# Kernel tuning notes

Measured on AMD Instinct MI355X. Metric: run time of the kernel, lower is better.

Reference implementation:

```python
import jax, jax.numpy as jnp
import numpy as np

B, T = 4096, 256
NX, NU, NY, NB, NA, H = 128, 16, 16, 32, 32, 256


def _lin(key, fan_in, fan_out):
    return jax.random.normal(key, (fan_in, fan_out), jnp.float32) / np.sqrt(fan_in)


def _mlp_res_params(key, din, dout):
    ks = jax.random.split(key, 4)
    return dict(
        rW=_lin(ks[0], din, dout), rb=jnp.zeros((dout,), jnp.float32),
        W1=_lin(ks[1], din, H), b1=jnp.zeros((H,), jnp.float32),
        W2=_lin(ks[2], H, H), b2=jnp.zeros((H,), jnp.float32),
        W3=_lin(ks[3], H, dout), b3=jnp.zeros((dout,), jnp.float32),
    )


def setup_inputs() -> dict:
    key = jax.random.key(0)
    k_up, k_yp, k_uf, k_enc, k_f, k_h = jax.random.split(key, 6)
    inp = {
        'upast': jax.random.normal(k_up, (B, NB, NU), jnp.float32),
        'ypast': jax.random.normal(k_yp, (B, NA, NY), jnp.float32),
        'ufuture': jax.random.normal(k_uf, (B, T, NU), jnp.float32),
    }
    enc = _mlp_res_params(k_enc, NB * NU + NA * NY, NX)
    f = _mlp_res_params(k_f, NX + NU, NX)
    h = _mlp_res_params(k_h, NX, NY)
    for name, p in (('enc', enc), ('f', f), ('h', h)):
        for k, v in p.items():
            inp[f'{name}_{k}'] = v
    return inp


def _mlp_res(x, rW, rb, W1, b1, W2, b2, W3, b3):
    # MLP_res_net: linear skip + 2-hidden-layer tanh MLP
    hid = jnp.tanh(x @ W1 + b1)
    hid = jnp.tanh(hid @ W2 + b2)
    return (x @ rW + rb) + (hid @ W3 + b3)


def reference(upast, ypast, ufuture,
              enc_rW, enc_rb, enc_W1, enc_b1, enc_W2, enc_b2, enc_W3, enc_b3,
              f_rW, f_rb, f_W1, f_b1, f_W2, f_b2, f_W3, f_b3,
              h_rW, h_rb, h_W1, h_b1, h_W2, h_b2, h_W3, h_b3):
    Bq, Tq = ufuture.shape[:2]
    # encoder: flatten+concat past windows -> x0 [B, nx]
    z = jnp.concatenate([upast.reshape(Bq, -1), ypast.reshape(Bq, -1)], axis=-1)
    x0 = _mlp_res(z, enc_rW, enc_rb, enc_W1, enc_b1, enc_W2, enc_b2, enc_W3, enc_b3)

    def step(x, u):
        xu = jnp.concatenate([x, u], axis=-1)
        x_next = _mlp_res(xu, f_rW, f_rb, f_W1, f_b1, f_W2, f_b2, f_W3, f_b3)
        return x_next, x  # store state BEFORE update (matches torch loop)

    _, xf = jax.lax.scan(step, x0, ufuture.swapaxes(0, 1))  # [T, B, nx]
    xf = xf.swapaxes(0, 1).reshape(Bq * Tq, -1)
    y = _mlp_res(xf, h_rW, h_rb, h_W1, h_b1, h_W2, h_b2, h_W3, h_b3)
    return y.reshape(Bq, Tq, -1)
```

## Files before the change

kernel.cpp:

```cpp
#include <hip/hip_runtime.h>
#include <stdint.h>


typedef __attribute__((ext_vector_type(8))) short s8v;
typedef __attribute__((ext_vector_type(8))) _Float16 h8v;
typedef __attribute__((ext_vector_type(4))) float f4v;

__device__ __forceinline__ f4v mfma16(s8v a, s8v b, f4v c) {
  return __builtin_amdgcn_mfma_f32_16x16x32_bf16(a, b, c, 0, 0, 0);
}
__device__ __forceinline__ f4v mfmaH(h8v a, h8v b, f4v c) {
  return __builtin_amdgcn_mfma_f32_16x16x32_f16(a, b, c, 0, 0, 0);
}
__device__ __forceinline__ f4v zero4() { return (f4v){0.f, 0.f, 0.f, 0.f}; }

__device__ __forceinline__ unsigned short f2b(float x) {
  unsigned int u = __builtin_bit_cast(unsigned int, x);
  u += 0x7fffu + ((u >> 16) & 1u);
  return (unsigned short)(u >> 16);
}
__device__ __forceinline__ float b2f(unsigned short h) {
  return __builtin_bit_cast(float, (unsigned int)h << 16);
}
__device__ __forceinline__ unsigned short f2h(float x) {
  return __builtin_bit_cast(unsigned short, (_Float16)x);
}
__device__ __forceinline__ float h2f(unsigned short h) {
  return (float)__builtin_bit_cast(_Float16, h);
}

__device__ __forceinline__ float tanhf_fast(float x) {
  x = fminf(15.f, fmaxf(-15.f, x));
  float e = __expf(2.f * x);
  return (e - 1.f) / (e + 1.f);
}

struct SwzDesc { const float* src; long woff; long dhi; long dlo; int K; int Kp; int N; int mode; };
struct SwzTable { SwzDesc d[12]; long tot_work; };

__global__ void swz_kernel(SwzTable tbl, unsigned short* __restrict__ dst) {
  long gid = (long)blockIdx.x * 256 + threadIdx.x;
  if (gid >= tbl.tot_work) return;
  int i = 11;
  while (i > 0 && gid < tbl.d[i].woff) --i;
  const SwzDesc m = tbl.d[i];
  long local = gid - m.woff;
  int j = (int)(local & 7);
// ... 106 lines not shown
    s8v al = *(const s8v*)(&h2l[c][kk * 32 + g * 8]);
    s8v bh = *(const s8v*)(W3h + (((long)w * 8 + kk) * 64 + l) * 8);
    s8v bl = *(const s8v*)(W3l + (((long)w * 8 + kk) * 64 + l) * 8);
    ac = mfma16(ah, bh, ac);
    ac = mfma16(al, bh, ac);
    ac = mfma16(ah, bl, ac);
  }
  for (int kk = 0; kk < 32; ++kk) {
    const int cb = kk * 32 + g * 8;
    const float* zp = (cb < 512) ? (upast + zrow + cb) : (ypast + zrow + (cb - 512));
    float4 z0 = *(const float4*)zp;
    float4 z1 = *(const float4*)(zp + 4);
    float zz[8] = {z0.x, z0.y, z0.z, z0.w, z1.x, z1.y, z1.z, z1.w};
    s8v ah, al;
#pragma unroll
    for (int q = 0; q < 8; ++q) {
      unsigned short hi = f2b(zz[q]);
      ah[q] = (short)hi; al[q] = (short)f2b(zz[q] - b2f(hi));
    }
    s8v bh = *(const s8v*)(rWh + (((long)w * 32 + kk) * 64 + l) * 8);
    s8v bl = *(const s8v*)(rWl + (((long)w * 32 + kk) * 64 + l) * 8);
    ac = mfma16(ah, bh, ac);
    ac = mfma16(al, bh, ac);
    ac = mfma16(ah, bl, ac);
  }
  {
    const float bias = b3[w * 16 + c] + rb[w * 16 + c];
#pragma unroll
    for (int j = 0; j < 4; ++j)
      xstate[(long)(b0 + g * 4 + j) * 128 + w * 16 + c] = ac[j] + bias;
  }
}

__global__ __launch_bounds__(512, 2)
void recur_kernel(const float* __restrict__ ufut,
                  const unsigned short* __restrict__ W1h, const unsigned short* __restrict__ W1l,
                  const unsigned short* __restrict__ W2h, const unsigned short* __restrict__ W2l,
                  const unsigned short* __restrict__ W3h, const unsigned short* __restrict__ W3l,
                  const unsigned short* __restrict__ rWh, const unsigned short* __restrict__ rWl,
                  const float* __restrict__ b1, const float* __restrict__ b2,
                  const float* __restrict__ b3, const float* __restrict__ rb,
                  float* __restrict__ xstate,
                  unsigned short* __restrict__ xfh, unsigned short* __restrict__ xfl,
                  int t0, int len) {
  __shared__ __align__(16) unsigned short xu_h[16][168], xu_l[16][168];
  __shared__ __align__(16) unsigned short hh[16][264], hl[16][264];
  __shared__ __align__(16) unsigned short w3h_l[32768];
  __shared__ __align__(16) unsigned short w3l_l[32768];
  const int tid = threadIdx.x;
  const int w = tid >> 6, l = tid & 63;
  const int c = l & 15, g = l >> 4;
  const int b0 = blockIdx.x << 4;

  h8v w1h_r[2][5], w1l_r[2][5], w2h_r[2][8], rwh_r[5], rwl_r[5];
#pragma unroll
  for (int ct = 0; ct < 2; ++ct) {
#pragma unroll
    for (int kk = 0; kk < 5; ++kk) {
      w1h_r[ct][kk] = *(const h8v*)(W1h + (((long)(2 * w + ct) * 5 + kk) * 64 + l) * 8);
      w1l_r[ct][kk] = *(const h8v*)(W1l + (((long)(2 * w + ct) * 5 + kk) * 64 + l) * 8);
    }
#pragma unroll
    for (int kk = 0; kk < 8; ++kk)
      w2h_r[ct][kk] = *(const h8v*)(W2h + (((long)(2 * w + ct) * 8 + kk) * 64 + l) * 8);
  }
#pragma unroll
  for (int kk = 0; kk < 5; ++kk) {
    rwh_r[kk] = *(const h8v*)(rWh + (((long)w * 5 + kk) * 64 + l) * 8);
    rwl_r[kk] = *(const h8v*)(rWl + (((long)w * 5 + kk) * 64 + l) * 8);
  }
  for (int i = tid; i < 4096; i += 512) {
    ((h8v*)w3h_l)[i] = ((const h8v*)W3h)[i];
    ((h8v*)w3l_l)[i] = ((const h8v*)W3l)[i];
  }

  const float bbA = b1[(2 * w + 0) * 16 + c], bbB = b1[(2 * w + 1) * 16 + c];
  const float cbA = b2[(2 * w + 0) * 16 + c], cbB = b2[(2 * w + 1) * 16 + c];
  const float dB  = b3[w * 16 + c] + rb[w * 16 + c];

  for (int idx = tid; idx < 2048; idx += 512) {
    int r = idx >> 7, cc = idx & 127;
    float x = xstate[(long)(b0 + r) * 128 + cc];
    _Float16 hi = (_Float16)x;
    xu_h[r][cc] = __builtin_bit_cast(unsigned short, hi);
    xu_l[r][cc] = f2h((x - (float)hi) * 2048.f);
  }
  for (int idx = tid; idx < 16 * 24; idx += 512) {
    int r = idx / 24, cc = 144 + (idx % 24);
    xu_h[r][cc] = 0; xu_l[r][cc] = 0;
  }
  __syncthreads();

  for (int tc = 0; tc < len; ++tc) {
    const int t = t0 + tc;
    h8v w2s[8];
#pragma unroll
    for (int kk = 0; kk < 8; ++kk)
      w2s[kk] = *(const h8v*)(W2l + (((long)(2 * w + 0) * 8 + kk) * 64 + l) * 8);
    if (tid < 256) {
      int r = tid >> 4, cc = tid & 15;
      float uv = ufut[((long)(b0 + r) * 256 + t) * 16 + cc];
      _Float16 hi = (_Float16)uv;
      xu_h[r][128 + cc] = __builtin_bit_cast(unsigned short, hi);
      xu_l[r][128 + cc] = f2h((uv - (float)hi) * 2048.f);
    }
    {
      int r = tid >> 5, cc0 = (tid & 31) * 4;
      long row = ((long)(b0 + r) * len + tc) * 128 + cc0;
      unsigned long long ph =
            (unsigned long long)xu_h[r][cc0 + 0]
          | ((unsigned long long)xu_h[r][cc0 + 1] << 16)
          | ((unsigned long long)xu_h[r][cc0 + 2] << 32)
          | ((unsigned long long)xu_h[r][cc0 + 3] << 48);
      unsigned long long pl =
            (unsigned long long)xu_l[r][cc0 + 0]
          | ((unsigned long long)xu_l[r][cc0 + 1] << 16)
          | ((unsigned long long)xu_l[r][cc0 + 2] << 32)
          | ((unsigned long long)xu_l[r][cc0 + 3] << 48);
      *(unsigned long long*)(xfh + row) = ph;
      *(unsigned long long*)(xfl + row) = pl;
    }
    __syncthreads();
    float v1s[2][4];
#pragma unroll
    for (int ct = 0; ct < 2; ++ct) {
      f4v t1 = zero4(), tl = zero4();
#pragma unroll
      for (int kk = 0; kk < 5; ++kk) {
        h8v ah = *(const h8v*)(&xu_h[c][kk * 32 + g * 8]);
        h8v al = *(const h8v*)(&xu_l[c][kk * 32 + g * 8]);
        t1 = mfmaH(ah, w1h_r[ct][kk], t1);
        tl = mfmaH(al, w1h_r[ct][kk], tl);
        tl = mfmaH(ah, w1l_r[ct][kk], tl);
      }
      const float bb = ct ? bbB : bbA;
#pragma unroll
      for (int j = 0; j < 4; ++j) v1s[ct][j] = t1[j] + tl[j] * 0x1p-11f + bb;
    }
#pragma unroll
    for (int ct = 0; ct < 2; ++ct)
#pragma unroll
      for (int j = 0; j < 4; ++j) {
        float tv = tanhf_fast(v1s[ct][j]);
        _Float16 hi = (_Float16)tv;
        hh[g * 4 + j][(2 * w + ct) * 16 + c] = __builtin_bit_cast(unsigned short, hi);
        hl[g * 4 + j][(2 * w + ct) * 16 + c] = f2h((tv - (float)hi) * 2048.f);
      }
    __syncthreads();
    float v2s[2][4];
#pragma unroll
    for (int ct = 0; ct < 2; ++ct) {
      f4v t1 = zero4(), tl = zero4();
#pragma unroll
      for (int kk = 0; kk < 8; ++kk) {
        h8v ah = *(const h8v*)(&hh[c][kk * 32 + g * 8]);
        h8v al = *(const h8v*)(&hl[c][kk * 32 + g * 8]);
        t1 = mfmaH(ah, w2h_r[ct][kk], t1);
        tl = mfmaH(al, w2h_r[ct][kk], tl);
        tl = mfmaH(ah, w2s[kk], tl);
        if (ct == 0)
          w2s[kk] = *(const h8v*)(W2l + (((long)(2 * w + 1) * 8 + kk) * 64 + l) * 8);
      }
      const float cb = ct ? cbB : cbA;
#pragma unroll
      for (int j = 0; j < 4; ++j) v2s[ct][j] = t1[j] + tl[j] * 0x1p-11f + cb;
    }
    __syncthreads();
#pragma unroll
    for (int ct = 0; ct < 2; ++ct)
#pragma unroll
      for (int j = 0; j < 4; ++j) {
        float tv = tanhf_fast(v2s[ct][j]);
        _Float16 hi = (_Float16)tv;
        hh[g * 4 + j][(2 * w + ct) * 16 + c] = __builtin_bit_cast(unsigned short, hi);
        hl[g * 4 + j][(2 * w + ct) * 16 + c] = f2h((tv - (float)hi) * 2048.f);
      }
    __syncthreads();
    {
      f4v t1 = zero4(), tl = zero4();
#pragma unroll
      for (int kk = 0; kk < 8; ++kk) {
        h8v ah = *(const h8v*)(&hh[c][kk * 32 + g * 8]);
        h8v al = *(const h8v*)(&hl[c][kk * 32 + g * 8]);
        h8v bh = *(const h8v*)(&w3h_l[((w * 8 + kk) * 64 + l) * 8]);
        h8v bl = *(const h8v*)(&w3l_l[((w * 8 + kk) * 64 + l) * 8]);
        t1 = mfmaH(ah, bh, t1);
        tl = mfmaH(al, bh, tl);
        tl = mfmaH(ah, bl, tl);
      }
#pragma unroll
      for (int kk = 0; kk < 5; ++kk) {
        h8v ah = *(const h8v*)(&xu_h[c][kk * 32 + g * 8]);
        h8v al = *(const h8v*)(&xu_l[c][kk * 32 + g * 8]);
        t1 = mfmaH(ah, rwh_r[kk], t1);
        tl = mfmaH(al, rwh_r[kk], tl);
        tl = mfmaH(ah, rwl_r[kk], tl);
      }
      __syncthreads();
#pragma unroll
      for (int j = 0; j < 4; ++j) {
        float xn = t1[j] + tl[j] * 0x1p-11f + dB;
        _Float16 hi = (_Float16)xn;
        xu_h[g * 4 + j][w * 16 + c] = __builtin_bit_cast(unsigned short, hi);
        xu_l[g * 4 + j][w * 16 + c] = f2h((xn - (float)hi) * 2048.f);
      }
    }
    __syncthreads();
  }
  for (int idx = tid; idx < 2048; idx += 512) {
    int r = idx >> 7, cc = idx & 127;
    xstate[(long)(b0 + r) * 128 + cc] = h2f(xu_h[r][cc]) + h2f(xu_l[r][cc]) * 0x1p-11f;
  }
}

__global__ __launch_bounds__(512, 2)
void hnet_kernel(const unsigned short* __restrict__ xfh, const unsigned short* __restrict__ xfl,
                 const unsigned short* __restrict__ W1, const unsigned short* __restrict__ W2,
                 const unsigned short* __restrict__ W3, const unsigned short* __restrict__ rW,
                 const float* __restrict__ b1, const float* __restrict__ b2,
                 const float* __restrict__ b3, const float* __restrict__ rb,
                 float* __restrict__ out, int t0, int len) {
  __shared__ __align__(16) unsigned short h1[64][264];
  __shared__ __align__(16) unsigned short h2[64][264];
  __shared__ float part[4][16][16];
  const int tid = threadIdx.x;
  const int w = tid >> 6, l = tid & 63;
  const int c = l & 15, g = l >> 4;
  const long row0 = (long)blockIdx.x * 64;

  {
    h8v w1f[2][4];
#pragma unroll
    for (int ct = 0; ct < 2; ++ct)
#pragma unroll
      for (int kk = 0; kk < 4; ++kk)
        w1f[ct][kk] = *(const h8v*)(W1 + (((long)(2 * w + ct) * 4 + kk) * 64 + l) * 8);
    const float bbA = b1[(2 * w + 0) * 16 + c], bbB = b1[(2 * w + 1) * 16 + c];
    for (int rt = 0; rt < 4; ++rt) {
      f4v t10 = zero4(), tl0 = zero4(), t11 = zero4(), tl1 = zero4();
#pragma unroll
      for (int kk = 0; kk < 4; ++kk) {
        h8v ah = *(const h8v*)(xfh + (row0 + rt * 16 + c) * 128 + kk * 32 + g * 8);
        h8v al = *(const h8v*)(xfl + (row0 + rt * 16 + c) * 128 + kk * 32 + g * 8);
        t10 = mfmaH(ah, w1f[0][kk], t10);
        tl0 = mfmaH(al, w1f[0][kk], tl0);
        t11 = mfmaH(ah, w1f[1][kk], t11);
        tl1 = mfmaH(al, w1f[1][kk], tl1);
      }
#pragma unroll
      for (int j = 0; j < 4; ++j) {
        h1[rt * 16 + g * 4 + j][(2 * w + 0) * 16 + c] =
            f2h(tanhf_fast(t10[j] + tl0[j] * 0x1p-11f + bbA));
        h1[rt * 16 + g * 4 + j][(2 * w + 1) * 16 + c] =
            f2h(tanhf_fast(t11[j] + tl1[j] * 0x1p-11f + bbB));
      }
    }
  }
  __syncthreads();
  {
    h8v w2f[2][8];
#pragma unroll
    for (int ct = 0; ct < 2; ++ct)
#pragma unroll
      for (int kk = 0; kk < 8; ++kk)
        w2f[ct][kk] = *(const h8v*)(W2 + (((long)(2 * w + ct) * 8 + kk) * 64 + l) * 8);
    const float bbA = b2[(2 * w + 0) * 16 + c], bbB = b2[(2 * w + 1) * 16 + c];
    for (int rt = 0; rt < 4; ++rt) {
      f4v a0 = zero4(), a1 = zero4();
#pragma unroll
      for (int kk = 0; kk < 8; ++kk) {
        h8v a = *(const h8v*)(&h1[rt * 16 + c][kk * 32 + g * 8]);
        a0 = mfmaH(a, w2f[0][kk], a0);
        a1 = mfmaH(a, w2f[1][kk], a1);
      }
#pragma unroll
      for (int j = 0; j < 4; ++j) {
        h2[rt * 16 + g * 4 + j][(2 * w + 0) * 16 + c] = f2h(tanhf_fast(a0[j] + bbA));
        h2[rt * 16 + g * 4 + j][(2 * w + 1) * 16 + c] = f2h(tanhf_fast(a1[j] + bbB));
      }
    }
  }
  __syncthreads();
  {
    const int rt = w & 3, kh = w >> 2;
    f4v t1 = zero4(), tl = zero4();
#pragma unroll
    for (int kk = 0; kk < 4; ++kk) {
      const int kkg = kh * 4 + kk;
      h8v a = *(const h8v*)(&h2[rt * 16 + c][kkg * 32 + g * 8]);
      h8v b = *(const h8v*)(W3 + ((long)(kkg * 64 + l)) * 8);
      t1 = mfmaH(a, b, t1);
    }
#pragma unroll
    for (int kk = 0; kk < 2; ++kk) {
      const int kkg = kh * 2 + kk;
      h8v ah = *(const h8v*)(xfh + (row0 + rt * 16 + c) * 128 + kkg * 32 + g * 8);
      h8v al = *(const h8v*)(xfl + (row0 + rt * 16 + c) * 128 + kkg * 32 + g * 8);
      h8v b = *(const h8v*)(rW + ((long)(kkg * 64 + l)) * 8);
      t1 = mfmaH(ah, b, t1);
      tl = mfmaH(al, b, tl);
    }
    float val[4];
#pragma unroll
    for (int j = 0; j < 4; ++j) val[j] = t1[j] + tl[j] * 0x1p-11f;
    if (w >= 4) {
#pragma unroll
      for (int j = 0; j < 4; ++j) part[rt][g * 4 + j][c] = val[j];
    }
    __syncthreads();
    if (w < 4) {
      const float bias = b3[c] + rb[c];
#pragma unroll
      for (int j = 0; j < 4; ++j) {
        const long grow = row0 + rt * 16 + g * 4 + j;
        const long bq = grow / len;
        const int tq = (int)(grow - bq * len);
        out[(bq * 256 + (t0 + tq)) * 16 + c] = val[j] + part[rt][g * 4 + j][c] + bias;
      }
    }
  }
}

extern "C" void kernel_launch(void* const* d_in, const int* in_sizes, int n_in,
                              void* d_out, int out_size, void* d_ws, size_t ws_size,
                              hipStream_t stream) {
  (void)in_sizes; (void)n_in; (void)out_size;
  const float* upast = (const float*)d_in[0];
  const float* ypast = (const float*)d_in[1];
  const float* ufut  = (const float*)d_in[2];
  const float* e_rW = (const float*)d_in[3];
  const float* e_rb = (const float*)d_in[4];
  const float* e_W1 = (const float*)d_in[5];
  const float* e_b1 = (const float*)d_in[6];
  const float* e_W2 = (const float*)d_in[7];
  const float* e_b2 = (const float*)d_in[8];
  const float* e_W3 = (const float*)d_in[9];
  const float* e_b3 = (const float*)d_in[10];
  const float* f_rW = (const float*)d_in[11];
  const float* f_rb = (const float*)d_in[12];
  const float* f_W1 = (const float*)d_in[13];
  const float* f_b1 = (const float*)d_in[14];
  const float* f_W2 = (const float*)d_in[15];
  const float* f_b2 = (const float*)d_in[16];
  const float* f_W3 = (const float*)d_in[17];
  const float* f_b3 = (const float*)d_in[18];
  const float* h_rW = (const float*)d_in[19];
  const float* h_rb = (const float*)d_in[20];
  const float* h_W1 = (const float*)d_in[21];
  const float* h_b1 = (const float*)d_in[22];
  const float* h_W2 = (const float*)d_in[23];
// ... 30 lines not shown
  unsigned short* wswz = (unsigned short*)d_ws;
  const long WSHORTS = HB + (offs[11] - offs[8]) + (long)Kps[11] * Ns[11];
  const size_t XOFF = ((size_t)WSHORTS * 2 + 4095) & ~(size_t)4095;
  float* xstate = (float*)((char*)d_ws + XOFF);
  const size_t XF0 = XOFF + (2u << 20);
  int c = 64;
  {
    long cmax = ((long)ws_size - (long)XF0) >> 21;
    if (cmax < c) c = (int)cmax;
    if (c < 1) c = 1;
  }
  unsigned short* xfh = (unsigned short*)((char*)d_ws + XF0);
  unsigned short* xfl = (unsigned short*)((char*)d_ws + XF0 + (size_t)c * 1048576);

  const unsigned short* eW1h = wswz + offs[0];          const unsigned short* eW1l = wswz + EA + offs[0];
  const unsigned short* eW2h = wswz + offs[1];          const unsigned short* eW2l = wswz + EA + offs[1];
  const unsigned short* eW3h = wswz + offs[2];          const unsigned short* eW3l = wswz + EA + offs[2];
  const unsigned short* erWh = wswz + offs[3];          const unsigned short* erWl = wswz + EA + offs[3];
  const unsigned short* fW1h = wswz + FB + 0;           const unsigned short* fW1l = wswz + FB + EB + 0;
  const unsigned short* fW2h = wswz + FB + 40960;       const unsigned short* fW2l = wswz + FB + EB + 40960;
  const unsigned short* fW3h = wswz + FB + 106496;      const unsigned short* fW3l = wswz + FB + EB + 106496;
  const unsigned short* frWh = wswz + FB + 139264;      const unsigned short* frWl = wswz + FB + EB + 139264;
  const unsigned short* hW1 = wswz + HB + 0;
  const unsigned short* hW2 = wswz + HB + 32768;
  const unsigned short* hW3 = wswz + HB + 98304;
  const unsigned short* hrW = wswz + HB + 102400;

  swz_kernel<<<(int)((tbl.tot_work + 255) / 256), 256, 0, stream>>>(tbl, wswz);
  enc_kernel<<<256, 512, 0, stream>>>(upast, ypast,
                                      eW1h, eW1l, eW2h, eW2l, eW3h, eW3l, erWh, erWl,
                                      e_b1, e_b2, e_b3, e_rb, xstate);
  for (int t0 = 0; t0 < 256; t0 += c) {
    int len = 256 - t0; if (len > c) len = c;
    recur_kernel<<<256, 512, 0, stream>>>(ufut, fW1h, fW1l, fW2h, fW2l, fW3h, fW3l,
                                          frWh, frWl, f_b1, f_b2, f_b3, f_rb,
                                          xstate, xfh, xfl, t0, len);
    hnet_kernel<<<64 * len, 512, 0, stream>>>(xfh, xfl, hW1, hW2, hW3, hrW,
                                              h_b1, h_b2, h_b3, h_rb, out, t0, len);
  }
}
```

Baseline: 2.920 ms.

## Double-buffer recurrent state and separate hidden buffers to cut barriers per step

The recurrent kernel now double-buffers the state tile and uses separate LDS buffers for the two hidden layers. This removes the intermediate __syncthreads calls, cutting the per-step barriers from five to three. The input u is loaded directly into registers as the last K-chunk instead of going through LDS. Both column tiles' MFMA chains are interleaved, with separate accumulators for independence. W2-low and W3-low are now streamed from global memory each step instead of being kept in registers or LDS, and launch bounds drop to 1 block per SM. Together these trade occupancy and extra global loads for fewer barriers and more instruction-level parallelism on the latency-bound sequential loop.

```diff
diff --git a/kernel.cpp b/kernel.cpp
--- a/kernel.cpp
+++ b/kernel.cpp
@@ -13,6 +13,12 @@
   return __builtin_amdgcn_mfma_f32_16x16x32_f16(a, b, c, 0, 0, 0);
 }
 __device__ __forceinline__ f4v zero4() { return (f4v){0.f, 0.f, 0.f, 0.f}; }
+__device__ __forceinline__ h8v zeroh8() {
+  h8v z;
+#pragma unroll
+  for (int q = 0; q < 8; ++q) z[q] = (_Float16)0.f;
+  return z;
+}
 
 __device__ __forceinline__ unsigned short f2b(float x) {
   unsigned int u = __builtin_bit_cast(unsigned int, x);
@@ -185,7 +191,7 @@
   }
 }
 
-__global__ __launch_bounds__(512, 2)
+__global__ __launch_bounds__(512, 1)
 void recur_kernel(const float* __restrict__ ufut,
                   const unsigned short* __restrict__ W1h, const unsigned short* __restrict__ W1l,
                   const unsigned short* __restrict__ W2h, const unsigned short* __restrict__ W2l,
@@ -196,10 +202,10 @@
                   float* __restrict__ xstate,
                   unsigned short* __restrict__ xfh, unsigned short* __restrict__ xfl,
                   int t0, int len) {
-  __shared__ __align__(16) unsigned short xu_h[16][168], xu_l[16][168];
-  __shared__ __align__(16) unsigned short hh[16][264], hl[16][264];
+  __shared__ __align__(16) unsigned short xu_h[2][16][136], xu_l[2][16][136];
+  __shared__ __align__(16) unsigned short h1h[16][264], h1l[16][264];
+  __shared__ __align__(16) unsigned short h2h[16][264], h2l[16][264];
   __shared__ __align__(16) unsigned short w3h_l[32768];
-  __shared__ __align__(16) unsigned short w3l_l[32768];
   const int tid = threadIdx.x;
   const int w = tid >> 6, l = tid & 63;
   const int c = l & 15, g = l >> 4;
@@ -222,10 +228,8 @@
     rwh_r[kk] = *(const h8v*)(rWh + (((long)w * 5 + kk) * 64 + l) * 8);
     rwl_r[kk] = *(const h8v*)(rWl + (((long)w * 5 + kk) * 64 + l) * 8);
   }
-  for (int i = tid; i < 4096; i += 512) {
+  for (int i = tid; i < 4096; i += 512)
     ((h8v*)w3h_l)[i] = ((const h8v*)W3h)[i];
-    ((h8v*)w3l_l)[i] = ((const h8v*)W3l)[i];
-  }
 
   const float bbA = b1[(2 * w + 0) * 16 + c], bbB = b1[(2 * w + 1) * 16 + c];
   const float cbA = b2[(2 * w + 0) * 16 + c], cbB = b2[(2 * w + 1) * 16 + c];
@@ -235,134 +239,139 @@
     int r = idx >> 7, cc = idx & 127;
     float x = xstate[(long)(b0 + r) * 128 + cc];
     _Float16 hi = (_Float16)x;
-    xu_h[r][cc] = __builtin_bit_cast(unsigned short, hi);
-    xu_l[r][cc] = f2h((x - (float)hi) * 2048.f);
-  }
-  for (int idx = tid; idx < 16 * 24; idx += 512) {
-    int r = idx / 24, cc = 144 + (idx % 24);
-    xu_h[r][cc] = 0; xu_l[r][cc] = 0;
+    xu_h[0][r][cc] = __builtin_bit_cast(unsigned short, hi);
+    xu_l[0][r][cc] = f2h((x - (float)hi) * 2048.f);
   }
   __syncthreads();
 
   for (int tc = 0; tc < len; ++tc) {
     const int t = t0 + tc;
-    h8v w2s[8];
-#pragma unroll
-    for (int kk = 0; kk < 8; ++kk)
-      w2s[kk] = *(const h8v*)(W2l + (((long)(2 * w + 0) * 8 + kk) * 64 + l) * 8);
-    if (tid < 256) {
-      int r = tid >> 4, cc = tid & 15;
-      float uv = ufut[((long)(b0 + r) * 256 + t) * 16 + cc];
-      _Float16 hi = (_Float16)uv;
-      xu_h[r][128 + cc] = __builtin_bit_cast(unsigned short, hi);
-      xu_l[r][128 + cc] = f2h((uv - (float)hi) * 2048.f);
+    const int cur = tc & 1;
+    h8v ah4 = zeroh8(), al4 = zeroh8();
+    if (g < 2) {
+      const float* up = ufut + ((long)(b0 + c) * 256 + t) * 16 + g * 8;
+      float4 u0 = *(const float4*)up;
+      float4 u1 = *(const float4*)(up + 4);
+      float uu[8] = {u0.x, u0.y, u0.z, u0.w, u1.x, u1.y, u1.z, u1.w};
+#pragma unroll
+      for (int q = 0; q < 8; ++q) {
+        _Float16 hi = (_Float16)uu[q];
+        ah4[q] = hi;
+        al4[q] = (_Float16)((uu[q] - (float)hi) * 2048.f);
+      }
     }
     {
       int r = tid >> 5, cc0 = (tid & 31) * 4;
       long row = ((long)(b0 + r) * len + tc) * 128 + cc0;
       unsigned long long ph =
-            (unsigned long long)xu_h[r][cc0 + 0]
-          | ((unsigned long long)xu_h[r][cc0 + 1] << 16)
-          | ((unsigned long long)xu_h[r][cc0 + 2] << 32)
-          | ((unsigned long long)xu_h[r][cc0 + 3] << 48);
+            (unsigned long long)xu_h[cur][r][cc0 + 0]
+          | ((unsigned long long)xu_h[cur][r][cc0 + 1] << 16)
+          | ((unsigned long long)xu_h[cur][r][cc0 + 2] << 32)
+          | ((unsigned long long)xu_h[cur][r][cc0 + 3] << 48);
       unsigned long long pl =
-            (unsigned long long)xu_l[r][cc0 + 0]
-          | ((unsigned long long)xu_l[r][cc0 + 1] << 16)
-          | ((unsigned long long)xu_l[r][cc0 + 2] << 32)
-          | ((unsigned long long)xu_l[r][cc0 + 3] << 48);
+            (unsigned long long)xu_l[cur][r][cc0 + 0]
+          | ((unsigned long long)xu_l[cur][r][cc0 + 1] << 16)
+          | ((unsigned long long)xu_l[cur][r][cc0 + 2] << 32)
+          | ((unsigned long long)xu_l[cur][r][cc0 + 3] << 48);
       *(unsigned long long*)(xfh + row) = ph;
       *(unsigned long long*)(xfl + row) = pl;
     }
-    __syncthreads();
-    float v1s[2][4];
-#pragma unroll
-    for (int ct = 0; ct < 2; ++ct) {
-      f4v t1 = zero4(), tl = zero4();
+    {
+      f4v p0 = zero4(), q0 = zero4(), p1 = zero4(), q1 = zero4();
 #pragma unroll
       for (int kk = 0; kk < 5; ++kk) {
-        h8v ah = *(const h8v*)(&xu_h[c][kk * 32 + g * 8]);
-        h8v al = *(const h8v*)(&xu_l[c][kk * 32 + g * 8]);
-        t1 = mfmaH(ah, w1h_r[ct][kk], t1);
-        tl = mfmaH(al, w1h_r[ct][kk], tl);
-        tl = mfmaH(ah, w1l_r[ct][kk], tl);
-      }
-      const float bb = ct ? bbB : bbA;
-#pragma unroll
-      for (int j = 0; j < 4; ++j) v1s[ct][j] = t1[j] + tl[j] * 0x1p-11f + bb;
-    }
-#pragma unroll
-    for (int ct = 0; ct < 2; ++ct)
+        h8v ah, al;
+        if (kk < 4) {
+          ah = *(const h8v*)(&xu_h[cur][c][kk * 32 + g * 8]);
+          al = *(const h8v*)(&xu_l[cur][c][kk * 32 + g * 8]);
+        } else { ah = ah4; al = al4; }
+        p0 = mfmaH(ah, w1h_r[0][kk], p0);
+        q0 = mfmaH(al, w1h_r[0][kk], q0);
+        q0 = mfmaH(ah, w1l_r[0][kk], q0);
+        p1 = mfmaH(ah, w1h_r[1][kk], p1);
+        q1 = mfmaH(al, w1h_r[1][kk], q1);
+        q1 = mfmaH(ah, w1l_r[1][kk], q1);
+      }
 #pragma unroll
       for (int j = 0; j < 4; ++j) {
-        float tv = tanhf_fast(v1s[ct][j]);
-        _Float16 hi = (_Float16)tv;
-        hh[g * 4 + j][(2 * w + ct) * 16 + c] = __builtin_bit_cast(unsigned short, hi);
-        hl[g * 4 + j][(2 * w + ct) * 16 + c] = f2h((tv - (float)hi) * 2048.f);
-      }
-    __syncthreads();
-    float v2s[2][4];
-#pragma unroll
-    for (int ct = 0; ct < 2; ++ct) {
-      f4v t1 = zero4(), tl = zero4();
-#pragma unroll
-      for (int kk = 0; kk < 8; ++kk) {
-        h8v ah = *(const h8v*)(&hh[c][kk * 32 + g * 8]);
-        h8v al = *(const h8v*)(&hl[c][kk * 32 + g * 8]);
-        t1 = mfmaH(ah, w2h_r[ct][kk], t1);
-        tl = mfmaH(al, w2h_r[ct][kk], tl);
-        tl = mfmaH(ah, w2s[kk], tl);
-        if (ct == 0)
-          w2s[kk] = *(const h8v*)(W2l + (((long)(2 * w + 1) * 8 + kk) * 64 + l) * 8);
-      }
-      const float cb = ct ? cbB : cbA;
-#pragma unroll
-      for (int j = 0; j < 4; ++j) v2s[ct][j] = t1[j] + tl[j] * 0x1p-11f + cb;
-    }
-    __syncthreads();
-#pragma unroll
-    for (int ct = 0; ct < 2; ++ct)
-#pragma unroll
-      for (int j = 0; j < 4; ++j) {
-        float tv = tanhf_fast(v2s[ct][j]);
-        _Float16 hi = (_Float16)tv;
-        hh[g * 4 + j][(2 * w + ct) * 16 + c] = __builtin_bit_cast(unsigned short, hi);
-        hl[g * 4 + j][(2 * w + ct) * 16 + c] = f2h((tv - (float)hi) * 2048.f);
-      }
+        float tA = tanhf_fast(p0[j] + q0[j] * 0x1p-11f + bbA);
+        float tB = tanhf_fast(p1[j] + q1[j] * 0x1p-11f + bbB);
+        _Float16 hA = (_Float16)tA, hB = (_Float16)tB;
+        h1h[g * 4 + j][(2 * w + 0) * 16 + c] = __builtin_bit_cast(unsigned short, hA);
+        h1l[g * 4 + j][(2 * w + 0) * 16 + c] = f2h((tA - (float)hA) * 2048.f);
+        h1h[g * 4 + j][(2 * w + 1) * 16 + c] = __builtin_bit_cast(unsigned short, hB);
+        h1l[g * 4 + j][(2 * w + 1) * 16 + c] = f2h((tB - (float)hB) * 2048.f);
+      }
+    }
     __syncthreads();
     {
-      f4v t1 = zero4(), tl = zero4();
+      f4v p0 = zero4(), q0 = zero4(), r0 = zero4();
+      f4v p1 = zero4(), q1 = zero4(), r1 = zero4();
 #pragma unroll
       for (int kk = 0; kk < 8; ++kk) {
-        h8v ah = *(const h8v*)(&hh[c][kk * 32 + g * 8]);
-        h8v al = *(const h8v*)(&hl[c][kk * 32 + g * 8]);
+        h8v ah = *(const h8v*)(&h1h[c][kk * 32 + g * 8]);
+        h8v al = *(const h8v*)(&h1l[c][kk * 32 + g * 8]);
+        h8v bl0 = *(const h8v*)(W2l + (((long)(2 * w + 0) * 8 + kk) * 64 + l) * 8);
+        h8v bl1 = *(const h8v*)(W2l + (((long)(2 * w + 1) * 8 + kk) * 64 + l) * 8);
+        p0 = mfmaH(ah, w2h_r[0][kk], p0);
+        q0 = mfmaH(al, w2h_r[0][kk], q0);
+        r0 = mfmaH(ah, bl0, r0);
+        p1 = mfmaH(ah, w2h_r[1][kk], p1);
+        q1 = mfmaH(al, w2h_r[1][kk], q1);
+        r1 = mfmaH(ah, bl1, r1);
+      }
+#pragma unroll
+      for (int j = 0; j < 4; ++j) {
+        float tA = tanhf_fast(p0[j] + (q0[j] + r0[j]) * 0x1p-11f + cbA);
+        float tB = tanhf_fast(p1[j] + (q1[j] + r1[j]) * 0x1p-11f + cbB);
+        _Float16 hA = (_Float16)tA, hB = (_Float16)tB;
+        h2h[g * 4 + j][(2 * w + 0) * 16 + c] = __builtin_bit_cast(unsigned short, hA);
+        h2l[g * 4 + j][(2 * w + 0) * 16 + c] = f2h((tA - (float)hA) * 2048.f);
+        h2h[g * 4 + j][(2 * w + 1) * 16 + c] = __builtin_bit_cast(unsigned short, hB);
+        h2l[g * 4 + j][(2 * w + 1) * 16 + c] = f2h((tB - (float)hB) * 2048.f);
+      }
+    }
+    __syncthreads();
+    {
+      f4v p = zero4(), q = zero4(), r = zero4();
+#pragma unroll
+      for (int kk = 0; kk < 8; ++kk) {
+        h8v ah = *(const h8v*)(&h2h[c][kk * 32 + g * 8]);
+        h8v al = *(const h8v*)(&h2l[c][kk * 32 + g * 8]);
         h8v bh = *(const h8v*)(&w3h_l[((w * 8 + kk) * 64 + l) * 8]);
-        h8v bl = *(const h8v*)(&w3l_l[((w * 8 + kk) * 64 + l) * 8]);
-        t1 = mfmaH(ah, bh, t1);
-        tl = mfmaH(al, bh, tl);
-        tl = mfmaH(ah, bl, tl);
+        h8v bl = *(const h8v*)(W3l + (((long)w * 8 + kk) * 64 + l) * 8);
+        p = mfmaH(ah, bh, p);
+        q = mfmaH(al, bh, q);
+        r = mfmaH(ah, bl, r);
       }
 #pragma unroll
       for (int kk = 0; kk < 5; ++kk) {
-        h8v ah = *(const h8v*)(&xu_h[c][kk * 32 + g * 8]);
-        h8v al = *(const h8v*)(&xu_l[c][kk * 32 + g * 8]);
-        t1 = mfmaH(ah, rwh_r[kk], t1);
-        tl = mfmaH(al, rwh_r[kk], tl);
-        tl = mfmaH(ah, rwl_r[kk], tl);
-      }
-      __syncthreads();
+        h8v ah, al;
+        if (kk < 4) {
+          ah = *(const h8v*)(&xu_h[cur][c][kk * 32 + g * 8]);
+          al = *(const h8v*)(&xu_l[cur][c][kk * 32 + g * 8]);
+        } else { ah = ah4; al = al4; }
+        p = mfmaH(ah, rwh_r[kk], p);
+        q = mfmaH(al, rwh_r[kk], q);
+        r = mfmaH(ah, rwl_r[kk], r);
+      }
 #pragma unroll
       for (int j = 0; j < 4; ++j) {
-        float xn = t1[j] + tl[j] * 0x1p-11f + dB;
+        float xn = p[j] + (q[j] + r[j]) * 0x1p-11f + dB;
         _Float16 hi = (_Float16)xn;
-        xu_h[g * 4 + j][w * 16 + c] = __builtin_bit_cast(unsigned short, hi);
-        xu_l[g * 4 + j][w * 16 + c] = f2h((xn - (float)hi) * 2048.f);
+        xu_h[cur ^ 1][g * 4 + j][w * 16 + c] = __builtin_bit_cast(unsigned short, hi);
+        xu_l[cur ^ 1][g * 4 + j][w * 16 + c] = f2h((xn - (float)hi) * 2048.f);
       }
     }
     __syncthreads();
   }
-  for (int idx = tid; idx < 2048; idx += 512) {
-    int r = idx >> 7, cc = idx & 127;
-    xstate[(long)(b0 + r) * 128 + cc] = h2f(xu_h[r][cc]) + h2f(xu_l[r][cc]) * 0x1p-11f;
+  {
+    const int fin = len & 1;
+    for (int idx = tid; idx < 2048; idx += 512) {
+      int r = idx >> 7, cc = idx & 127;
+      xstate[(long)(b0 + r) * 128 + cc] =
+          h2f(xu_h[fin][r][cc]) + h2f(xu_l[fin][r][cc]) * 0x1p-11f;
+    }
   }
 }
 
```

New measurement: 3.891 ms. +33.3%, slower.

## Widen recurrence kernel to 16 waves with split output/skip GEMMs

Applied to the files above, without the earlier changes.

The recurrent step kernel moves from 512 to 1024 threads. Each wave now owns one 16-column tile of the hidden layers instead of two, and the final layer is split so waves 0-7 compute the W3 product while waves 8-15 compute the skip projection into a shared partial buffer. Low-part weights are streamed from global/L2 every step through an opaque zero offset instead of being held in registers or LDS. The next step's input is prefetched during the combine phase, which removes one barrier per step. The aim is shorter per-step latency through more parallel waves, at the cost of more global weight traffic and one more LDS reduction.

```diff
diff --git a/kernel.cpp b/kernel.cpp
--- a/kernel.cpp
+++ b/kernel.cpp
@@ -185,7 +185,7 @@
   }
 }
 
-__global__ __launch_bounds__(512, 2)
+__global__ __launch_bounds__(1024, 4)
 void recur_kernel(const float* __restrict__ ufut,
                   const unsigned short* __restrict__ W1h, const unsigned short* __restrict__ W1l,
                   const unsigned short* __restrict__ W2h, const unsigned short* __restrict__ W2l,
@@ -197,172 +197,161 @@
                   unsigned short* __restrict__ xfh, unsigned short* __restrict__ xfl,
                   int t0, int len) {
   __shared__ __align__(16) unsigned short xu_h[16][168], xu_l[16][168];
-  __shared__ __align__(16) unsigned short hh[16][264], hl[16][264];
+  __shared__ __align__(16) unsigned short h1h[16][264], h1l[16][264];
+  __shared__ __align__(16) unsigned short h2h[16][264], h2l[16][264];
   __shared__ __align__(16) unsigned short w3h_l[32768];
-  __shared__ __align__(16) unsigned short w3l_l[32768];
+  __shared__ __align__(16) unsigned short rwh_l[20480];
+  __shared__ __align__(16) float part[16][136];
   const int tid = threadIdx.x;
   const int w = tid >> 6, l = tid & 63;
   const int c = l & 15, g = l >> 4;
   const int b0 = blockIdx.x << 4;
 
-  h8v w1h_r[2][5], w1l_r[2][5], w2h_r[2][8], rwh_r[5], rwl_r[5];
-#pragma unroll
-  for (int ct = 0; ct < 2; ++ct) {
-#pragma unroll
-    for (int kk = 0; kk < 5; ++kk) {
-      w1h_r[ct][kk] = *(const h8v*)(W1h + (((long)(2 * w + ct) * 5 + kk) * 64 + l) * 8);
-      w1l_r[ct][kk] = *(const h8v*)(W1l + (((long)(2 * w + ct) * 5 + kk) * 64 + l) * 8);
-    }
-#pragma unroll
-    for (int kk = 0; kk < 8; ++kk)
-      w2h_r[ct][kk] = *(const h8v*)(W2h + (((long)(2 * w + ct) * 8 + kk) * 64 + l) * 8);
-  }
-#pragma unroll
-  for (int kk = 0; kk < 5; ++kk) {
-    rwh_r[kk] = *(const h8v*)(rWh + (((long)w * 5 + kk) * 64 + l) * 8);
-    rwl_r[kk] = *(const h8v*)(rWl + (((long)w * 5 + kk) * 64 + l) * 8);
-  }
-  for (int i = tid; i < 4096; i += 512) {
-    ((h8v*)w3h_l)[i] = ((const h8v*)W3h)[i];
-    ((h8v*)w3l_l)[i] = ((const h8v*)W3l)[i];
-  }
-
-  const float bbA = b1[(2 * w + 0) * 16 + c], bbB = b1[(2 * w + 1) * 16 + c];
-  const float cbA = b2[(2 * w + 0) * 16 + c], cbB = b2[(2 * w + 1) * 16 + c];
-  const float dB  = b3[w * 16 + c] + rb[w * 16 + c];
-
-  for (int idx = tid; idx < 2048; idx += 512) {
+  h8v w1h_r[5], w2h_r[8];
+#pragma unroll
+  for (int kk = 0; kk < 5; ++kk)
+    w1h_r[kk] = *(const h8v*)(W1h + (((long)w * 5 + kk) * 64 + l) * 8);
+#pragma unroll
+  for (int kk = 0; kk < 8; ++kk)
+    w2h_r[kk] = *(const h8v*)(W2h + (((long)w * 8 + kk) * 64 + l) * 8);
+
+  for (int i = tid; i < 4096; i += 1024) ((h8v*)w3h_l)[i] = ((const h8v*)W3h)[i];
+  for (int i = tid; i < 2560; i += 1024) ((h8v*)rwh_l)[i] = ((const h8v*)rWh)[i];
+
+  const float bb = b1[w * 16 + c];
+  const float cb = b2[w * 16 + c];
+  const float dB = (w < 8) ? (b3[w * 16 + c] + rb[w * 16 + c]) : 0.f;
+
+  for (int idx = tid; idx < 2048; idx += 1024) {
     int r = idx >> 7, cc = idx & 127;
     float x = xstate[(long)(b0 + r) * 128 + cc];
     _Float16 hi = (_Float16)x;
     xu_h[r][cc] = __builtin_bit_cast(unsigned short, hi);
     xu_l[r][cc] = f2h((x - (float)hi) * 2048.f);
   }
-  for (int idx = tid; idx < 16 * 24; idx += 512) {
-    int r = idx / 24, cc = 144 + (idx % 24);
-    xu_h[r][cc] = 0; xu_l[r][cc] = 0;
+  if (tid < 256) {
+    int r = tid >> 4, cc = tid & 15;
+    xu_h[r][144 + cc] = 0; xu_l[r][144 + cc] = 0;
+    float uv = ufut[((long)(b0 + r) * 256 + t0) * 16 + cc];
+    _Float16 hi = (_Float16)uv;
+    xu_h[r][128 + cc] = __builtin_bit_cast(unsigned short, hi);
+    xu_l[r][128 + cc] = f2h((uv - (float)hi) * 2048.f);
   }
   __syncthreads();
 
   for (int tc = 0; tc < len; ++tc) {
     const int t = t0 + tc;
-    h8v w2s[8];
-#pragma unroll
-    for (int kk = 0; kk < 8; ++kk)
-      w2s[kk] = *(const h8v*)(W2l + (((long)(2 * w + 0) * 8 + kk) * 64 + l) * 8);
-    if (tid < 256) {
-      int r = tid >> 4, cc = tid & 15;
-      float uv = ufut[((long)(b0 + r) * 256 + t) * 16 + cc];
+    long lz = 0;
+    asm volatile("" : "+s"(lz));
+    const unsigned short* W1ls = W1l + lz;
+    const unsigned short* W2ls = W2l + lz;
+    const unsigned short* W3ls = W3l + lz;
+    const unsigned short* rWls = rWl + lz;
+
+    {
+      int r = tid >> 6, cc0 = (tid & 63) * 2;
+      long row = ((long)(b0 + r) * len + tc) * 128 + cc0;
+      *(unsigned int*)(xfh + row) =
+          (unsigned int)xu_h[r][cc0] | ((unsigned int)xu_h[r][cc0 + 1] << 16);
+      *(unsigned int*)(xfl + row) =
+          (unsigned int)xu_l[r][cc0] | ((unsigned int)xu_l[r][cc0 + 1] << 16);
+    }
+    {
+      f4v p = zero4(), q = zero4();
+#pragma unroll
+      for (int kk = 0; kk < 5; ++kk) {
+        h8v ah = *(const h8v*)(&xu_h[c][kk * 32 + g * 8]);
+        h8v al = *(const h8v*)(&xu_l[c][kk * 32 + g * 8]);
+        h8v bl = *(const h8v*)(W1ls + (((long)w * 5 + kk) * 64 + l) * 8);
+        p = mfmaH(ah, w1h_r[kk], p);
+        q = mfmaH(al, w1h_r[kk], q);
+        q = mfmaH(ah, bl, q);
+      }
+#pragma unroll
+      for (int j = 0; j < 4; ++j) {
+        float tv = tanhf_fast(p[j] + q[j] * 0x1p-11f + bb);
+        _Float16 hi = (_Float16)tv;
+        h1h[g * 4 + j][w * 16 + c] = __builtin_bit_cast(unsigned short, hi);
+        h1l[g * 4 + j][w * 16 + c] = f2h((tv - (float)hi) * 2048.f);
+      }
+    }
+    __syncthreads();
+    {
+      f4v p = zero4(), q = zero4(), r2 = zero4();
+#pragma unroll
+      for (int kk = 0; kk < 8; ++kk) {
+        h8v ah = *(const h8v*)(&h1h[c][kk * 32 + g * 8]);
+        h8v al = *(const h8v*)(&h1l[c][kk * 32 + g * 8]);
+        h8v bl = *(const h8v*)(W2ls + (((long)w * 8 + kk) * 64 + l) * 8);
+        p = mfmaH(ah, w2h_r[kk], p);
+        q = mfmaH(al, w2h_r[kk], q);
+        r2 = mfmaH(ah, bl, r2);
+      }
+#pragma unroll
+      for (int j = 0; j < 4; ++j) {
+        float tv = tanhf_fast(p[j] + (q[j] + r2[j]) * 0x1p-11f + cb);
+        _Float16 hi = (_Float16)tv;
+        h2h[g * 4 + j][w * 16 + c] = __builtin_bit_cast(unsigned short, hi);
+        h2l[g * 4 + j][w * 16 + c] = f2h((tv - (float)hi) * 2048.f);
+      }
+    }
+    __syncthreads();
+    float pv[4], qv[4];
+    if (w < 8) {
+      f4v p = zero4(), q = zero4(), r2 = zero4();
+#pragma unroll
+      for (int kk = 0; kk < 8; ++kk) {
+        h8v ah = *(const h8v*)(&h2h[c][kk * 32 + g * 8]);
+        h8v al = *(const h8v*)(&h2l[c][kk * 32 + g * 8]);
+        h8v bh = *(const h8v*)(&w3h_l[(((long)w * 8 + kk) * 64 + l) * 8]);
+        h8v bl = *(const h8v*)(W3ls + (((long)w * 8 + kk) * 64 + l) * 8);
+        p = mfmaH(ah, bh, p);
+        q = mfmaH(al, bh, q);
+        r2 = mfmaH(ah, bl, r2);
+      }
+#pragma unroll
+      for (int j = 0; j < 4; ++j) { pv[j] = p[j]; qv[j] = q[j] + r2[j]; }
+    } else {
+      const int cw = w - 8;
+      f4v p = zero4(), q = zero4();
+#pragma unroll
+      for (int kk = 0; kk < 5; ++kk) {
+        h8v ah = *(const h8v*)(&xu_h[c][kk * 32 + g * 8]);
+        h8v al = *(const h8v*)(&xu_l[c][kk * 32 + g * 8]);
+        h8v bh = *(const h8v*)(&rwh_l[(((long)cw * 5 + kk) * 64 + l) * 8]);
+        h8v bl = *(const h8v*)(rWls + (((long)cw * 5 + kk) * 64 + l) * 8);
+        p = mfmaH(ah, bh, p);
+        q = mfmaH(al, bh, q);
+        q = mfmaH(ah, bl, q);
+      }
+#pragma unroll
+      for (int j = 0; j < 4; ++j)
+        part[g * 4 + j][cw * 16 + c] = p[j] + q[j] * 0x1p-11f;
+    }
+    __syncthreads();
+    if (w < 8) {
+#pragma unroll
+      for (int j = 0; j < 4; ++j) {
+        float xn = pv[j] + qv[j] * 0x1p-11f + part[g * 4 + j][w * 16 + c] + dB;
+        _Float16 hi = (_Float16)xn;
+        xu_h[g * 4 + j][w * 16 + c] = __builtin_bit_cast(unsigned short, hi);
+        xu_l[g * 4 + j][w * 16 + c] = f2h((xn - (float)hi) * 2048.f);
+      }
+    } else if (w < 12) {
+      int idx = (w - 8) * 64 + l;
+      int r = idx >> 4, cc = idx & 15;
+      int tt = (t + 1 < 256) ? (t + 1) : 255;
+      float uv = ufut[((long)(b0 + r) * 256 + tt) * 16 + cc];
       _Float16 hi = (_Float16)uv;
       xu_h[r][128 + cc] = __builtin_bit_cast(unsigned short, hi);
       xu_l[r][128 + cc] = f2h((uv - (float)hi) * 2048.f);
     }
-    {
-      int r = tid >> 5, cc0 = (tid & 31) * 4;
-      long row = ((long)(b0 + r) * len + tc) * 128 + cc0;
-      unsigned long long ph =
-            (unsigned long long)xu_h[r][cc0 + 0]
-          | ((unsigned long long)xu_h[r][cc0 + 1] << 16)
-          | ((unsigned long long)xu_h[r][cc0 + 2] << 32)
-          | ((unsigned long long)xu_h[r][cc0 + 3] << 48);
-      unsigned long long pl =
-            (unsigned long long)xu_l[r][cc0 + 0]
-          | ((unsigned long long)xu_l[r][cc0 + 1] << 16)
-          | ((unsigned long long)xu_l[r][cc0 + 2] << 32)
-          | ((unsigned long long)xu_l[r][cc0 + 3] << 48);
-      *(unsigned long long*)(xfh + row) = ph;
-      *(unsigned long long*)(xfl + row) = pl;
-    }
     __syncthreads();
-    float v1s[2][4];
-#pragma unroll
-    for (int ct = 0; ct < 2; ++ct) {
-      f4v t1 = zero4(), tl = zero4();
-#pragma unroll
-      for (int kk = 0; kk < 5; ++kk) {
-        h8v ah = *(const h8v*)(&xu_h[c][kk * 32 + g * 8]);
-        h8v al = *(const h8v*)(&xu_l[c][kk * 32 + g * 8]);
-        t1 = mfmaH(ah, w1h_r[ct][kk], t1);
-        tl = mfmaH(al, w1h_r[ct][kk], tl);
-        tl = mfmaH(ah, w1l_r[ct][kk], tl);
-      }
-      const float bb = ct ? bbB : bbA;
-#pragma unroll
-      for (int j = 0; j < 4; ++j) v1s[ct][j] = t1[j] + tl[j] * 0x1p-11f + bb;
-    }
-#pragma unroll
-    for (int ct = 0; ct < 2; ++ct)
-#pragma unroll
-      for (int j = 0; j < 4; ++j) {
-        float tv = tanhf_fast(v1s[ct][j]);
-        _Float16 hi = (_Float16)tv;
-        hh[g * 4 + j][(2 * w + ct) * 16 + c] = __builtin_bit_cast(unsigned short, hi);
-        hl[g * 4 + j][(2 * w + ct) * 16 + c] = f2h((tv - (float)hi) * 2048.f);
-      }
-    __syncthreads();
-    float v2s[2][4];
-#pragma unroll
-    for (int ct = 0; ct < 2; ++ct) {
-      f4v t1 = zero4(), tl = zero4();
-#pragma unroll
-      for (int kk = 0; kk < 8; ++kk) {
-        h8v ah = *(const h8v*)(&hh[c][kk * 32 + g * 8]);
-        h8v al = *(const h8v*)(&hl[c][kk * 32 + g * 8]);
-        t1 = mfmaH(ah, w2h_r[ct][kk], t1);
-        tl = mfmaH(al, w2h_r[ct][kk], tl);
-        tl = mfmaH(ah, w2s[kk], tl);
-        if (ct == 0)
-          w2s[kk] = *(const h8v*)(W2l + (((long)(2 * w + 1) * 8 + kk) * 64 + l) * 8);
-      }
-      const float cb = ct ? cbB : cbA;
-#pragma unroll
-      for (int j = 0; j < 4; ++j) v2s[ct][j] = t1[j] + tl[j] * 0x1p-11f + cb;
-    }
-    __syncthreads();
-#pragma unroll
-    for (int ct = 0; ct < 2; ++ct)
-#pragma unroll
-      for (int j = 0; j < 4; ++j) {
-        float tv = tanhf_fast(v2s[ct][j]);
-        _Float16 hi = (_Float16)tv;
-        hh[g * 4 + j][(2 * w + ct) * 16 + c] = __builtin_bit_cast(unsigned short, hi);
-        hl[g * 4 + j][(2 * w + ct) * 16 + c] = f2h((tv - (float)hi) * 2048.f);
-      }
-    __syncthreads();
-    {
-      f4v t1 = zero4(), tl = zero4();
-#pragma unroll
-      for (int kk = 0; kk < 8; ++kk) {
-        h8v ah = *(const h8v*)(&hh[c][kk * 32 + g * 8]);
-        h8v al = *(const h8v*)(&hl[c][kk * 32 + g * 8]);
-        h8v bh = *(const h8v*)(&w3h_l[((w * 8 + kk) * 64 + l) * 8]);
-        h8v bl = *(const h8v*)(&w3l_l[((w * 8 + kk) * 64 + l) * 8]);
-        t1 = mfmaH(ah, bh, t1);
-        tl = mfmaH(al, bh, tl);
-        tl = mfmaH(ah, bl, tl);
-      }
-#pragma unroll
-      for (int kk = 0; kk < 5; ++kk) {
-        h8v ah = *(const h8v*)(&xu_h[c][kk * 32 + g * 8]);
-        h8v al = *(const h8v*)(&xu_l[c][kk * 32 + g * 8]);
-        t1 = mfmaH(ah, rwh_r[kk], t1);
-        tl = mfmaH(al, rwh_r[kk], tl);
-        tl = mfmaH(ah, rwl_r[kk], tl);
-      }
-      __syncthreads();
-#pragma unroll
-      for (int j = 0; j < 4; ++j) {
-        float xn = t1[j] + tl[j] * 0x1p-11f + dB;
-        _Float16 hi = (_Float16)xn;
-        xu_h[g * 4 + j][w * 16 + c] = __builtin_bit_cast(unsigned short, hi);
-        xu_l[g * 4 + j][w * 16 + c] = f2h((xn - (float)hi) * 2048.f);
-      }
-    }
-    __syncthreads();
-  }
-  for (int idx = tid; idx < 2048; idx += 512) {
+  }
+  for (int idx = tid; idx < 2048; idx += 1024) {
     int r = idx >> 7, cc = idx & 127;
-    xstate[(long)(b0 + r) * 128 + cc] = h2f(xu_h[r][cc]) + h2f(xu_l[r][cc]) * 0x1p-11f;
+    xstate[(long)(b0 + r) * 128 + cc] =
+        h2f(xu_h[r][cc]) + h2f(xu_l[r][cc]) * 0x1p-11f;
   }
 }
 
@@ -565,9 +554,9 @@
                                       e_b1, e_b2, e_b3, e_rb, xstate);
   for (int t0 = 0; t0 < 256; t0 += c) {
     int len = 256 - t0; if (len > c) len = c;
-    recur_kernel<<<256, 512, 0, stream>>>(ufut, fW1h, fW1l, fW2h, fW2l, fW3h, fW3l,
-                                          frWh, frWl, f_b1, f_b2, f_b3, f_rb,
-                                          xstate, xfh, xfl, t0, len);
+    recur_kernel<<<256, 1024, 0, stream>>>(ufut, fW1h, fW1l, fW2h, fW2l, fW3h, fW3l,
+                                           frWh, frWl, f_b1, f_b2, f_b3, f_rb,
+                                           xstate, xfh, xfl, t0, len);
     hnet_kernel<<<64 * len, 512, 0, stream>>>(xfh, xfl, hW1, hW2, hW3, hrW,
                                               h_b1, h_b2, h_b3, h_rb, out, t0, len);
   }
```

New measurement: 3.186 ms. 9.1% more time.

## Make hnet kernel persistent and keep its weights resident in registers and LDS

Applied to the files above, without the earlier changes.

The output-network kernel now launches a fixed grid of 256 blocks that loop over row tiles, instead of one block per 64-row tile. W1 and the even column tiles of W2 are loaded once into registers, and the odd W2 tiles are staged once into a 64 KB shared-memory buffer. This removes the per-tile reloading of weight fragments from global memory. In exchange, shared-memory use rises to about 136 KB per block, which limits each CU to one resident block and leaves less latency hiding. Parallelism is also capped at 256 blocks.

```diff
diff --git a/kernel.cpp b/kernel.cpp
--- a/kernel.cpp
+++ b/kernel.cpp
@@ -375,100 +375,108 @@
                  float* __restrict__ out, int t0, int len) {
   __shared__ __align__(16) unsigned short h1[64][264];
   __shared__ __align__(16) unsigned short h2[64][264];
+  __shared__ __align__(16) unsigned short w2odd[32768];
   __shared__ float part[4][16][16];
   const int tid = threadIdx.x;
   const int w = tid >> 6, l = tid & 63;
   const int c = l & 15, g = l >> 4;
-  const long row0 = (long)blockIdx.x * 64;
-
-  {
-    h8v w1f[2][4];
-#pragma unroll
-    for (int ct = 0; ct < 2; ++ct)
-#pragma unroll
-      for (int kk = 0; kk < 4; ++kk)
-        w1f[ct][kk] = *(const h8v*)(W1 + (((long)(2 * w + ct) * 4 + kk) * 64 + l) * 8);
-    const float bbA = b1[(2 * w + 0) * 16 + c], bbB = b1[(2 * w + 1) * 16 + c];
-    for (int rt = 0; rt < 4; ++rt) {
-      f4v t10 = zero4(), tl0 = zero4(), t11 = zero4(), tl1 = zero4();
+
+  h8v w1f[2][4], w2f0[8];
+#pragma unroll
+  for (int ct = 0; ct < 2; ++ct)
+#pragma unroll
+    for (int kk = 0; kk < 4; ++kk)
+      w1f[ct][kk] = *(const h8v*)(W1 + (((long)(2 * w + ct) * 4 + kk) * 64 + l) * 8);
+#pragma unroll
+  for (int kk = 0; kk < 8; ++kk)
+    w2f0[kk] = *(const h8v*)(W2 + (((long)(2 * w + 0) * 8 + kk) * 64 + l) * 8);
+  for (int i = tid; i < 4096; i += 512) {
+    int wq = i >> 9, rem = i & 511, kk = rem >> 6, ll = rem & 63;
+    ((h8v*)w2odd)[i] = *(const h8v*)(W2 + (((long)(2 * wq + 1) * 8 + kk) * 64 + ll) * 8);
+  }
+  const float bbA1 = b1[(2 * w + 0) * 16 + c], bbB1 = b1[(2 * w + 1) * 16 + c];
+  const float bbA2 = b2[(2 * w + 0) * 16 + c], bbB2 = b2[(2 * w + 1) * 16 + c];
+  __syncthreads();
+
+  const int ntiles = 64 * len;
+  for (int tile = blockIdx.x; tile < ntiles; tile += 256) {
+    const long row0 = (long)tile * 64;
+    {
+      for (int rt = 0; rt < 4; ++rt) {
+        f4v t10 = zero4(), tl0 = zero4(), t11 = zero4(), tl1 = zero4();
+#pragma unroll
+        for (int kk = 0; kk < 4; ++kk) {
+          h8v ah = *(const h8v*)(xfh + (row0 + rt * 16 + c) * 128 + kk * 32 + g * 8);
+          h8v al = *(const h8v*)(xfl + (row0 + rt * 16 + c) * 128 + kk * 32 + g * 8);
+          t10 = mfmaH(ah, w1f[0][kk], t10);
+          tl0 = mfmaH(al, w1f[0][kk], tl0);
+          t11 = mfmaH(ah, w1f[1][kk], t11);
+          tl1 = mfmaH(al, w1f[1][kk], tl1);
+        }
+#pragma unroll
+        for (int j = 0; j < 4; ++j) {
+          h1[rt * 16 + g * 4 + j][(2 * w + 0) * 16 + c] =
+              f2h(tanhf_fast(t10[j] + tl0[j] * 0x1p-11f + bbA1));
+          h1[rt * 16 + g * 4 + j][(2 * w + 1) * 16 + c] =
+              f2h(tanhf_fast(t11[j] + tl1[j] * 0x1p-11f + bbB1));
+        }
+      }
+    }
+    __syncthreads();
+    {
+      for (int rt = 0; rt < 4; ++rt) {
+        f4v a0 = zero4(), a1 = zero4();
+#pragma unroll
+        for (int kk = 0; kk < 8; ++kk) {
+          h8v a = *(const h8v*)(&h1[rt * 16 + c][kk * 32 + g * 8]);
+          h8v b1f = *(const h8v*)(&w2odd[(((long)w * 8 + kk) * 64 + l) * 8]);
+          a0 = mfmaH(a, w2f0[kk], a0);
+          a1 = mfmaH(a, b1f, a1);
+        }
+#pragma unroll
+        for (int j = 0; j < 4; ++j) {
+          h2[rt * 16 + g * 4 + j][(2 * w + 0) * 16 + c] = f2h(tanhf_fast(a0[j] + bbA2));
+          h2[rt * 16 + g * 4 + j][(2 * w + 1) * 16 + c] = f2h(tanhf_fast(a1[j] + bbB2));
+        }
+      }
+    }
+    __syncthreads();
+    {
+      const int rt = w & 3, kh = w >> 2;
+      f4v t1 = zero4(), tl = zero4();
 #pragma unroll
       for (int kk = 0; kk < 4; ++kk) {
-        h8v ah = *(const h8v*)(xfh + (row0 + rt * 16 + c) * 128 + kk * 32 + g * 8);
-        h8v al = *(const h8v*)(xfl + (row0 + rt * 16 + c) * 128 + kk * 32 + g * 8);
-        t10 = mfmaH(ah, w1f[0][kk], t10);
-        tl0 = mfmaH(al, w1f[0][kk], tl0);
-        t11 = mfmaH(ah, w1f[1][kk], t11);
-        tl1 = mfmaH(al, w1f[1][kk], tl1);
-      }
-#pragma unroll
-      for (int j = 0; j < 4; ++j) {
-        h1[rt * 16 + g * 4 + j][(2 * w + 0) * 16 + c] =
-            f2h(tanhf_fast(t10[j] + tl0[j] * 0x1p-11f + bbA));
-        h1[rt * 16 + g * 4 + j][(2 * w + 1) * 16 + c] =
-            f2h(tanhf_fast(t11[j] + tl1[j] * 0x1p-11f + bbB));
-      }
-    }
-  }
-  __syncthreads();
-  {
-    h8v w2f[2][8];
-#pragma unroll
-    for (int ct = 0; ct < 2; ++ct)
-#pragma unroll
-      for (int kk = 0; kk < 8; ++kk)
-        w2f[ct][kk] = *(const h8v*)(W2 + (((long)(2 * w + ct) * 8 + kk) * 64 + l) * 8);
-    const float bbA = b2[(2 * w + 0) * 16 + c], bbB = b2[(2 * w + 1) * 16 + c];
-    for (int rt = 0; rt < 4; ++rt) {
-      f4v a0 = zero4(), a1 = zero4();
-#pragma unroll
-      for (int kk = 0; kk < 8; ++kk) {
-        h8v a = *(const h8v*)(&h1[rt * 16 + c][kk * 32 + g * 8]);
-        a0 = mfmaH(a, w2f[0][kk], a0);
-        a1 = mfmaH(a, w2f[1][kk], a1);
-      }
-#pragma unroll
-      for (int j = 0; j < 4; ++j) {
-        h2[rt * 16 + g * 4 + j][(2 * w + 0) * 16 + c] = f2h(tanhf_fast(a0[j] + bbA));
-        h2[rt * 16 + g * 4 + j][(2 * w + 1) * 16 + c] = f2h(tanhf_fast(a1[j] + bbB));
-      }
-    }
-  }
-  __syncthreads();
-  {
-    const int rt = w & 3, kh = w >> 2;
-    f4v t1 = zero4(), tl = zero4();
-#pragma unroll
-    for (int kk = 0; kk < 4; ++kk) {
-      const int kkg = kh * 4 + kk;
-      h8v a = *(const h8v*)(&h2[rt * 16 + c][kkg * 32 + g * 8]);
-      h8v b = *(const h8v*)(W3 + ((long)(kkg * 64 + l)) * 8);
-      t1 = mfmaH(a, b, t1);
-    }
-#pragma unroll
-    for (int kk = 0; kk < 2; ++kk) {
-      const int kkg = kh * 2 + kk;
-      h8v ah = *(const h8v*)(xfh + (row0 + rt * 16 + c) * 128 + kkg * 32 + g * 8);
-      h8v al = *(const h8v*)(xfl + (row0 + rt * 16 + c) * 128 + kkg * 32 + g * 8);
-      h8v b = *(const h8v*)(rW + ((long)(kkg * 64 + l)) * 8);
-      t1 = mfmaH(ah, b, t1);
-      tl = mfmaH(al, b, tl);
-    }
-    float val[4];
-#pragma unroll
-    for (int j = 0; j < 4; ++j) val[j] = t1[j] + tl[j] * 0x1p-11f;
-    if (w >= 4) {
-#pragma unroll
-      for (int j = 0; j < 4; ++j) part[rt][g * 4 + j][c] = val[j];
-    }
-    __syncthreads();
-    if (w < 4) {
-      const float bias = b3[c] + rb[c];
-#pragma unroll
-      for (int j = 0; j < 4; ++j) {
-        const long grow = row0 + rt * 16 + g * 4 + j;
-        const long bq = grow / len;
-        const int tq = (int)(grow - bq * len);
-        out[(bq * 256 + (t0 + tq)) * 16 + c] = val[j] + part[rt][g * 4 + j][c] + bias;
+        const int kkg = kh * 4 + kk;
+        h8v a = *(const h8v*)(&h2[rt * 16 + c][kkg * 32 + g * 8]);
+        h8v b = *(const h8v*)(W3 + ((long)(kkg * 64 + l)) * 8);
+        t1 = mfmaH(a, b, t1);
+      }
+#pragma unroll
+      for (int kk = 0; kk < 2; ++kk) {
+        const int kkg = kh * 2 + kk;
+        h8v ah = *(const h8v*)(xfh + (row0 + rt * 16 + c) * 128 + kkg * 32 + g * 8);
+        h8v al = *(const h8v*)(xfl + (row0 + rt * 16 + c) * 128 + kkg * 32 + g * 8);
+        h8v b = *(const h8v*)(rW + ((long)(kkg * 64 + l)) * 8);
+        t1 = mfmaH(ah, b, t1);
+        tl = mfmaH(al, b, tl);
+      }
+      float val[4];
+#pragma unroll
+      for (int j = 0; j < 4; ++j) val[j] = t1[j] + tl[j] * 0x1p-11f;
+      if (w >= 4) {
+#pragma unroll
+        for (int j = 0; j < 4; ++j) part[rt][g * 4 + j][c] = val[j];
+      }
+      __syncthreads();
+      if (w < 4) {
+        const float bias = b3[c] + rb[c];
+#pragma unroll
+        for (int j = 0; j < 4; ++j) {
+          const long grow = row0 + rt * 16 + g * 4 + j;
+          const long bq = grow / len;
+          const int tq = (int)(grow - bq * len);
+          out[(bq * 256 + (t0 + tq)) * 16 + c] = val[j] + part[rt][g * 4 + j][c] + bias;
+        }
       }
     }
   }
@@ -568,7 +576,7 @@
     recur_kernel<<<256, 512, 0, stream>>>(ufut, fW1h, fW1l, fW2h, fW2l, fW3h, fW3l,
                                           frWh, frWl, f_b1, f_b2, f_b3, f_rb,
                                           xstate, xfh, xfl, t0, len);
-    hnet_kernel<<<64 * len, 512, 0, stream>>>(xfh, xfl, hW1, hW2, hW3, hrW,
-                                              h_b1, h_b2, h_b3, h_rb, out, t0, len);
-  }
-}
+    hnet_kernel<<<256, 512, 0, stream>>>(xfh, xfl, hW1, hW2, hW3, hrW,
+                                         h_b1, h_b2, h_b3, h_rb, out, t0, len);
+  }
+}
```

Result: no change. 2.974 ms (+1.8%).
